# Kernel optimization log

Hardware: AMD Instinct MI355X
Metric: run time of the kernel (lower is better)

The kernel has to match this reference:

```python
import jax, jax.numpy as jnp
import numpy as np

B, S, T = 4, 512, 512
D, F, L, H, V = 512, 2048, 6, 8, 32000
HD = D // H


def setup_inputs() -> dict:
    key = jax.random.key(0)
    ks = list(jax.random.split(key, 16))
    it = iter(ks)

    def w(shape, scale=0.02):
        return jax.random.normal(next(it), shape, jnp.float32) * scale

    enc_in = jax.random.randint(next(it), (B, S), 0, V, dtype=jnp.int32)
    dec_in = jax.random.randint(next(it), (B, T), 0, V, dtype=jnp.int32)

    # sinusoidal positional encoding (make_sine_pos_encoding)
    pos = np.arange(S)[:, None].astype(np.float32)
    i = np.arange(D)[None, :].astype(np.float32)
    angle = pos / np.power(10000.0, (2.0 * np.floor(i / 2.0)) / D)
    pe = np.zeros((S, D), np.float32)
    pe[:, 0::2] = np.sin(angle[:, 0::2])
    pe[:, 1::2] = np.cos(angle[:, 1::2])

    return {
        "enc_in": enc_in,
        "dec_in": dec_in,
        "e_embed": w((V, D)),
        "d_embed": w((V, D)),
        "pos_enc": jnp.asarray(pe),
        "enc_mha_W": w((L, 4, D, D)),      # q,k,v,out
        "enc_mha_b": jnp.zeros((L, 4, D), jnp.float32),
        "enc_ln_g": jnp.ones((L, 2, D), jnp.float32),
        "enc_ln_b": jnp.zeros((L, 2, D), jnp.float32),
        "enc_ffn_W1": w((L, D, F)),
        "enc_ffn_b1": jnp.zeros((L, F), jnp.float32),
        "enc_ffn_W2": w((L, F, D)),
        "enc_ffn_b2": jnp.zeros((L, D), jnp.float32),
        "dec_mha_W": w((L, 8, D, D)),      # self q,k,v,out then cross q,k,v,out
        "dec_mha_b": jnp.zeros((L, 8, D), jnp.float32),
        "dec_ln_g": jnp.ones((L, 3, D), jnp.float32),
        "dec_ln_b": jnp.zeros((L, 3, D), jnp.float32),
        "dec_ffn_W1": w((L, D, F)),
        "dec_ffn_b1": jnp.zeros((L, F), jnp.float32),
        "dec_ffn_W2": w((L, F, D)),
        "dec_ffn_b2": jnp.zeros((L, D), jnp.float32),
    }


def _layer_norm(x, g, b, eps=1e-6):
    m = jnp.mean(x, axis=-1, keepdims=True)
    v = jnp.mean(jnp.square(x - m), axis=-1, keepdims=True)
    return (x - m) * jax.lax.rsqrt(v + eps) * g + b


def _split_heads(x):
    b, n, _ = x.shape
    return x.reshape(b, n, H, HD).transpose(0, 2, 1, 3)  # b h n d


def _mha(xq, xkv, W, b, mask):
    # W: [>=4, D, D] slice of (q,k,v,out); mask: broadcastable to [b,h,nq,nk]
    q = _split_heads(xq @ W[0] + b[0])
    k = _split_heads(xkv @ W[1] + b[1])
    v = _split_heads(xkv @ W[2] + b[2])
    s = jnp.einsum('bhqd,bhkd->bhqk', q, k) / jnp.sqrt(jnp.float32(HD))
    s = s + mask * (-1e9)
    a = jax.nn.softmax(s, axis=-1)
    o = jnp.einsum('bhqk,bhkd->bhqd', a, v)
    o = o.transpose(0, 2, 1, 3).reshape(xq.shape[0], xq.shape[1], D)
    return o @ W[3] + b[3]


def _forward(enc_in, dec_in, e_embed, d_embed, pos_enc,
             enc_mha_W, enc_mha_b, enc_ln_g, enc_ln_b,
             enc_ffn_W1, enc_ffn_b1, enc_ffn_W2, enc_ffn_b2,
             dec_mha_W, dec_mha_b, dec_ln_g, dec_ln_b,
             dec_ffn_W1, dec_ffn_b1, dec_ffn_W2, dec_ffn_b2):
    # masks: 1.0 where attention is blocked
    enc_pad = (enc_in == 0).astype(jnp.float32)[:, None, None, :]   # [B,1,1,S]
    dec_pad = (dec_in == 0).astype(jnp.float32)[:, None, None, :]   # [B,1,1,T]
    la = jnp.triu(jnp.ones((T, T), jnp.float32), k=1)[None, None]   # [1,1,T,T]
    look_ahead = jnp.maximum(la, dec_pad)                           # [B,1,T,T]

    scale = jnp.float32(D) ** 0.5
    e = e_embed[enc_in] * scale + pos_enc[None, :S]
    d = d_embed[dec_in] * scale + pos_enc[None, :T]

    for l in range(L):
        y = _mha(e, e, enc_mha_W[l], enc_mha_b[l], enc_pad)
        e = _layer_norm(e + y, enc_ln_g[l, 0], enc_ln_b[l, 0])
        y = jax.nn.relu(e @ enc_ffn_W1[l] + enc_ffn_b1[l]) @ enc_ffn_W2[l] + enc_ffn_b2[l]
        e = _layer_norm(e + y, enc_ln_g[l, 1], enc_ln_b[l, 1])

    for l in range(L):
        y = _mha(d, d, dec_mha_W[l, 0:4], dec_mha_b[l, 0:4], look_ahead)
        d = _layer_norm(d + y, dec_ln_g[l, 0], dec_ln_b[l, 0])
        y = _mha(d, e, dec_mha_W[l, 4:8], dec_mha_b[l, 4:8], enc_pad)
        d = _layer_norm(d + y, dec_ln_g[l, 1], dec_ln_b[l, 1])
        y = jax.nn.relu(d @ dec_ffn_W1[l] + dec_ffn_b1[l]) @ dec_ffn_W2[l] + dec_ffn_b2[l]
        d = _layer_norm(d + y, dec_ln_g[l, 2], dec_ln_b[l, 2])

    return d @ d_embed.T  # [B,T,V] logits


def reference(enc_in, dec_in, e_embed, d_embed, pos_enc,
              enc_mha_W, enc_mha_b, enc_ln_g, enc_ln_b,
              enc_ffn_W1, enc_ffn_b1, enc_ffn_W2, enc_ffn_b2,
              dec_mha_W, dec_mha_b, dec_ln_g, dec_ln_b,
              dec_ffn_W1, dec_ffn_b1, dec_ffn_W2, dec_ffn_b2):
    return _forward(enc_in, dec_in, e_embed, d_embed, pos_enc,
                    enc_mha_W, enc_mha_b, enc_ln_g, enc_ln_b,
                    enc_ffn_W1, enc_ffn_b1, enc_ffn_W2, enc_ffn_b2,
                    dec_mha_W, dec_mha_b, dec_ln_g, dec_ln_b,
                    dec_ffn_W1, dec_ffn_b1, dec_ffn_W2, dec_ffn_b2)
```

## Files before the change

kernel.cpp:

```cpp
#include <hip/hip_runtime.h>
#include <hip/hip_bf16.h>
#include <math.h>

#define B_ 4
#define S_ 512
#define D_ 512
#define F_ 2048
#define L_ 6
#define H_ 8
#define V_ 32000

typedef unsigned short u16;
typedef __attribute__((ext_vector_type(8))) short bhalf8;
typedef __attribute__((ext_vector_type(4))) float f32x4;

__device__ __forceinline__ u16 f2b(float v) {
    unsigned x = __builtin_bit_cast(unsigned, v);
    return (u16)((x + 0x7FFFu + ((x >> 16) & 1u)) >> 16);
}

#define GLD16(g, l) __builtin_amdgcn_global_load_lds( \
    (const __attribute__((address_space(1))) void*)(g), \
    (__attribute__((address_space(3))) void*)(l), 16, 0, 0)

__device__ __forceinline__ float redmax16(float v) {
    #pragma unroll
    for (int m = 1; m < 16; m <<= 1) v = fmaxf(v, __shfl_xor(v, m));
    return v;
}
__device__ __forceinline__ float redsum16(float v) {
    #pragma unroll
    for (int m = 1; m < 16; m <<= 1) v += __shfl_xor(v, m);
    return v;
}

template<int NWR, int NWC, int WM, int WN, int OUT, int RELU, int MLOOP,
         int SPLITA, int XMAJOR, int NT, int VTT, int SWZ>
__global__ __launch_bounds__(NWR * NWC * 64)
void mfma_gemm(const u16* __restrict__ A, const u16* __restrict__ A2, int acut,
               const u16* __restrict__ B,
               const float* __restrict__ bias, void* __restrict__ Cv,
               int K, int lda, int ldb, int ldc,
               u16* __restrict__ vtp, int vc0)
{
    constexpr int BM = NWR * WM, BN = NWC * WN;
    constexpr int NW = NWR * NWC;
    constexpr int CH_A = BM / 16, CH_B = BN / 16, CH = CH_A + CH_B;
    constexpr int NI = WM / 16, NJ = WN / 16;

    __shared__ u16 As[2][BM * 32];
    __shared__ u16 Bs[2][BN * 32];
    __shared__ u16 TT[VTT ? 64 * 72 : 8];

    const int tid = threadIdx.x;
    const int wid = tid >> 6, lane = tid & 63;
    const int wrow = wid / NWC, wcol = wid % NWC;
    long bn, bmbase;
    if (SWZ) {
        long b0 = blockIdx.x;
        long per = (long)gridDim.x >> 3;
        long w = (b0 & 7) * per + (b0 >> 3);
        bn = (w >> 4) * BN;
        bmbase = w & 15;
    } else {
        bn = (XMAJOR ? (long)blockIdx.y : (long)blockIdx.x) * BN;
        bmbase = (XMAJOR ? (long)blockIdx.x : (long)blockIdx.y);
    }
    const int r4 = lane >> 2, c4 = lane & 3;
    const int l15 = lane & 15, l4 = lane >> 4;

    const u16* Ause = (SPLITA && bn >= acut) ? A2 : A;

    #pragma unroll 1
    for (int mi = 0; mi < MLOOP; ++mi) {
        const long bm = (bmbase * MLOOP + mi) * BM;

        f32x4 acc[NI][NJ];
        #pragma unroll
        for (int i = 0; i < NI; ++i)
            #pragma unroll
            for (int j = 0; j < NJ; ++j)
                acc[i][j] = (f32x4){0.f, 0.f, 0.f, 0.f};

        #pragma unroll
        for (int t = 0; t < CH / NW; ++t) {
            int c = wid + t * NW;
            if (c < CH_A) {
                GLD16(Ause + (bm + c * 16 + r4) * (long)lda + c4 * 8,
                      &As[0][c * 512 + lane * 8]);
            } else {
                int cb = c - CH_A;
                GLD16(B + (bn + cb * 16 + r4) * (long)ldb + c4 * 8,
                      &Bs[0][cb * 512 + lane * 8]);
            }
        }

        for (int k0 = 0; k0 < K; k0 += 32) {
            const int cur = (k0 >> 5) & 1;
            __syncthreads();
            if (k0 + 32 < K) {
                const int kn = k0 + 32;
                #pragma unroll
                for (int t = 0; t < CH / NW; ++t) {
                    int c = wid + t * NW;
                    if (c < CH_A) {
                        GLD16(Ause + (bm + c * 16 + r4) * (long)lda + kn + c4 * 8,
                              &As[cur ^ 1][c * 512 + lane * 8]);
                    } else {
                        int cb = c - CH_A;
                        GLD16(B + (bn + cb * 16 + r4) * (long)ldb + kn + c4 * 8,
                              &Bs[cur ^ 1][cb * 512 + lane * 8]);
                    }
                }
            }
            bhalf8 af[NI], bfr[NJ];
            #pragma unroll
            for (int i = 0; i < NI; ++i)
                af[i] = *(const bhalf8*)&As[cur][(wrow * WM + i * 16 + l15) * 32 + l4 * 8];
            #pragma unroll
            for (int j = 0; j < NJ; ++j)
                bfr[j] = *(const bhalf8*)&Bs[cur][(wcol * WN + j * 16 + l15) * 32 + l4 * 8];
            #pragma unroll
            for (int i = 0; i < NI; ++i)
                #pragma unroll
                for (int j = 0; j < NJ; ++j)
                    acc[i][j] = __builtin_amdgcn_mfma_f32_16x16x32_bf16(af[i], bfr[j], acc[i][j], 0, 0, 0);
        }

        if (VTT && vtp != nullptr && bn >= vc0) {
            #pragma unroll
            for (int j = 0; j < NJ; ++j) {
                const int c = wcol * WN + j * 16 + l15;
                const float bv = bias ? bias[bn + c] : 0.f;
                #pragma unroll
                for (int i = 0; i < NI; ++i) {
                    const int rw = wrow * WM + i * 16 + (l4 << 2);
                    #pragma unroll
                    for (int r = 0; r < 4; ++r)
                        TT[c * 72 + rw + r] = f2b(acc[i][j][r] + bv);
                }
            }
            __syncthreads();
            {
                const int c = tid >> 1, hh = tid & 1;
                const u16* src = &TT[c * 72 + hh * 32];
                u16* dst = &vtp[(bn - vc0 + c) * 2048 + bm + hh * 32];
                #pragma unroll
                for (int p = 0; p < 4; ++p)
                    *(uint4*)(dst + p * 8) = *(const uint4*)(src + p * 8);
            }
            __syncthreads();
            continue;
        }

        float* Cf = (float*)Cv;
        u16*   Cb = (u16*)Cv;
        const int rowb = wrow * WM + (l4 << 2);
        const int colb = wcol * WN + l15;
        #pragma unroll
        for (int j = 0; j < NJ; ++j) {
            const long gc = bn + colb + j * 16;
            const float bv = bias ? bias[gc] : 0.f;
            #pragma unroll
            for (int i = 0; i < NI; ++i) {
                const long gr = bm + rowb + i * 16;
                #pragma unroll
                for (int r = 0; r < 4; ++r) {
                    float v = acc[i][j][r] + bv;
                    if (RELU) v = fmaxf(v, 0.f);
                    if (OUT == 0) {
                        if (NT) __builtin_nontemporal_store(v, &Cf[(gr + r) * (long)ldc + gc]);
                        else    Cf[(gr + r) * (long)ldc + gc] = v;
                    } else {
                        Cb[(gr + r) * (long)ldc + gc] = f2b(v);
                    }
                }
            }
        }
    }
}

__global__ __launch_bounds__(512)
void gemm_ln_kernel(const u16* __restrict__ A, const u16* __restrict__ B,
                    const float* __restrict__ bias,
                    float* __restrict__ x, u16* __restrict__ xb,
                    const float* __restrict__ g, const float* __restrict__ bb,
                    int K)
{
    __shared__ u16 As[16 * 32];
    __shared__ u16 Bs[512 * 32];
    __shared__ float red[2][16][8];
    __shared__ float mv[2][16];

    const int tid = threadIdx.x, w = tid >> 6, lane = tid & 63;
    const int l15 = lane & 15, l4 = lane >> 4;
    const int r4 = lane >> 2, c4 = lane & 3;
    const long bm = (long)blockIdx.x * 16;

    f32x4 acc[4];
    #pragma unroll
    for (int j = 0; j < 4; ++j) acc[j] = (f32x4){0.f, 0.f, 0.f, 0.f};

    for (int k0 = 0; k0 < K; k0 += 32) {
        #pragma unroll
        for (int t = 0; t < 5; ++t) {
            int c = w + t * 8;
            if (c < 33) {
                if (c == 0) {
                    GLD16(A + (bm + r4) * (long)K + k0 + c4 * 8, As + lane * 8);
                } else {
                    GLD16(B + ((c - 1) * 16 + r4) * (long)K + k0 + c4 * 8,
                          Bs + (c - 1) * 512 + lane * 8);
                }
            }
        }
        __syncthreads();
        bhalf8 af = *(const bhalf8*)&As[l15 * 32 + l4 * 8];
        #pragma unroll
        for (int j = 0; j < 4; ++j) {
            bhalf8 bf = *(const bhalf8*)&Bs[(w * 64 + j * 16 + l15) * 32 + l4 * 8];
            acc[j] = __builtin_amdgcn_mfma_f32_16x16x32_bf16(af, bf, acc[j], 0, 0, 0);
        }
        __syncthreads();
    }

    float vbuf[4][4], s[4] = {0, 0, 0, 0}, s2[4] = {0, 0, 0, 0};
    #pragma unroll
    for (int j = 0; j < 4; ++j) {
        int col = w * 64 + j * 16 + l15;
        float bv = bias[col];
        #pragma unroll
        for (int r = 0; r < 4; ++r) {
            int row = l4 * 4 + r;
            float v = acc[j][r] + bv + x[(bm + row) * 512 + col];
            vbuf[j][r] = v;
            s[r] += v; s2[r] += v * v;
        }
    }
    #pragma unroll
    for (int r = 0; r < 4; ++r) { s[r] = redsum16(s[r]); s2[r] = redsum16(s2[r]); }
    if (l15 == 0) {
        #pragma unroll
        for (int r = 0; r < 4; ++r) {
            red[0][l4 * 4 + r][w] = s[r];
            red[1][l4 * 4 + r][w] = s2[r];
        }
    }
    __syncthreads();
    if (tid < 16) {
        float S = 0.f, S2 = 0.f;
        #pragma unroll
        for (int q = 0; q < 8; ++q) { S += red[0][tid][q]; S2 += red[1][tid][q]; }
        float mean = S * (1.f / 512.f);
        float var = S2 * (1.f / 512.f) - mean * mean;
        mv[0][tid] = mean;
        mv[1][tid] = rsqrtf(var + 1e-6f);
    }
    __syncthreads();
    #pragma unroll
    for (int j = 0; j < 4; ++j) {
        int col = w * 64 + j * 16 + l15;
        float gg = g[col], bbv = bb[col];
        #pragma unroll
        for (int r = 0; r < 4; ++r) {
            int row = l4 * 4 + r;
            float o = (vbuf[j][r] - mv[0][row]) * mv[1][row] * gg + bbv;
            x[(bm + row) * 512 + col] = o;
            xb[(bm + row) * 512 + col] = f2b(o);
        }
    }
}

template<int CAUSAL>
__global__ __launch_bounds__(256)
void flash_kernel(const u16* __restrict__ Qp, int ldq,
                  const u16* __restrict__ Kp, int ldk,
                  const u16* __restrict__ Vt,
                  const int* __restrict__ tok,
                  u16* __restrict__ Op)
{
    __shared__ u16 QS[64 * 64];
    __shared__ u16 KS[2][64 * 64];
    __shared__ u16 VS[2][64 * 64];
    __shared__ u16 PS[4 * 16 * 64];
    __shared__ float MK[512];

    const int tid = threadIdx.x, lane = tid & 63, w = tid >> 6;
    const int l15 = lane & 15, l4 = lane >> 4;
    const int qb = blockIdx.x, bh = blockIdx.y;
    const int b = bh >> 3, h = bh & 7;

    const u16* Q = Qp + (long)(b * 512 + qb * 64) * ldq + h * 64;
    const u16* K = Kp + (long)(b * 512) * ldk + h * 64;
    const u16* V = Vt + (long)(h * 64) * 2048 + b * 512;
    u16* O = Op + (long)(b * 512 + qb * 64) * 512 + h * 64;

    {
        int t0 = tok[b * 512 + tid];
        int t1 = tok[b * 512 + 256 + tid];
        MK[tid]       = (t0 == 0) ? -1e9f : 0.f;
        MK[tid + 256] = (t1 == 0) ? -1e9f : 0.f;
    }
    const int r = tid >> 3;
    const int c = (tid & 7) ^ (r & 7);
    {
        GLD16(Q + (long)r * ldq + c * 8,        QS + tid * 8);
        GLD16(Q + (long)(r + 32) * ldq + c * 8, QS + 2048 + tid * 8);
        GLD16(K + (long)r * ldk + c * 8,              KS[0] + tid * 8);
        GLD16(K + (long)(32 + r) * ldk + c * 8,       KS[0] + 2048 + tid * 8);
        GLD16(V + (long)r * 2048 + c * 8,             VS[0] + tid * 8);
        GLD16(V + (long)(r + 32) * 2048 + c * 8,      VS[0] + 2048 + tid * 8);
    }
    __syncthreads();

    bhalf8 qa[2];
    #pragma unroll
    for (int kc = 0; kc < 2; ++kc) {
        int row = w * 16 + l15;
        qa[kc] = *(const bhalf8*)&QS[row * 64 + (((kc * 4 + l4) ^ (row & 7)) << 3)];
    }

    f32x4 oacc[4];
    float mrun[4], lrun[4];
    #pragma unroll
    for (int j = 0; j < 4; ++j) oacc[j] = (f32x4){0.f, 0.f, 0.f, 0.f};
    #pragma unroll
    for (int rr = 0; rr < 4; ++rr) { mrun[rr] = -1e30f; lrun[rr] = 0.f; }

    const int tmax = CAUSAL ? qb : 7;

    for (int t = 0; t <= tmax; ++t) {
        const int cur = t & 1;
        if (t < tmax) {
            const int tn = t + 1;
            GLD16(K + (long)(tn * 64 + r) * ldk + c * 8,        KS[cur ^ 1] + tid * 8);
            GLD16(K + (long)(tn * 64 + 32 + r) * ldk + c * 8,   KS[cur ^ 1] + 2048 + tid * 8);
            GLD16(V + (long)r * 2048 + tn * 64 + c * 8,         VS[cur ^ 1] + tid * 8);
            GLD16(V + (long)(r + 32) * 2048 + tn * 64 + c * 8,  VS[cur ^ 1] + 2048 + tid * 8);
        }
        f32x4 sac[4];
        #pragma unroll
        for (int jj = 0; jj < 4; ++jj) sac[jj] = (f32x4){0.f, 0.f, 0.f, 0.f};
        bhalf8 kf[4][2];
        #pragma unroll
        for (int jj = 0; jj < 4; ++jj)
            #pragma unroll
            for (int kc = 0; kc < 2; ++kc) {
                int row = jj * 16 + l15;
                kf[jj][kc] = *(const bhalf8*)&KS[cur][row * 64 + (((kc * 4 + l4) ^ (row & 7)) << 3)];
            }
        #pragma unroll
        for (int jj = 0; jj < 4; ++jj)
            #pragma unroll
            for (int kc = 0; kc < 2; ++kc)
                sac[jj] = __builtin_amdgcn_mfma_f32_16x16x32_bf16(qa[kc], kf[jj][kc], sac[jj], 0, 0, 0);

        #pragma unroll
        for (int jj = 0; jj < 4; ++jj) {
            float mk = MK[t * 64 + jj * 16 + l15];
            #pragma unroll
            for (int rr = 0; rr < 4; ++rr) {
                float mk2 = mk;
                if (CAUSAL && t == qb) {
                    int col = t * 64 + jj * 16 + l15;
                    int qr = qb * 64 + w * 16 + l4 * 4 + rr;
                    if (col > qr) mk2 = -1e9f;
                }
                sac[jj][rr] = sac[jj][rr] * 0.125f + mk2;
            }
        }
        #pragma unroll
        for (int rr = 0; rr < 4; ++rr) {
            float mx = fmaxf(fmaxf(sac[0][rr], sac[1][rr]), fmaxf(sac[2][rr], sac[3][rr]));
            mx = redmax16(mx);
            float mnew = fmaxf(mrun[rr], mx);
            float alpha = __expf(mrun[rr] - mnew);
            float sum = 0.f;
            int row_p = l4 * 4 + rr;
            #pragma unroll
            for (int jj = 0; jj < 4; ++jj) {
                float pv = __expf(sac[jj][rr] - mnew);
                sum += pv;
                int kv = jj * 16 + l15;
                PS[w * 1024 + row_p * 64 + ((((kv >> 3) ^ (row_p & 7)) << 3) | (kv & 7))] = f2b(pv);
            }
            sum = redsum16(sum);
            lrun[rr] = lrun[rr] * alpha + sum;
            mrun[rr] = mnew;
            #pragma unroll
            for (int jd = 0; jd < 4; ++jd) oacc[jd][rr] *= alpha;
        }
        bhalf8 pa[2], vf[4][2];
        #pragma unroll
        for (int kc = 0; kc < 2; ++kc) {
            int row = l15;
            pa[kc] = *(const bhalf8*)&PS[w * 1024 + row * 64 + (((kc * 4 + l4) ^ (row & 7)) << 3)];
        }
        #pragma unroll
        for (int jd = 0; jd < 4; ++jd)
            #pragma unroll
            for (int kc = 0; kc < 2; ++kc) {
                int row = jd * 16 + l15;
                vf[jd][kc] = *(const bhalf8*)&VS[cur][row * 64 + (((kc * 4 + l4) ^ (row & 7)) << 3)];
            }
        #pragma unroll
        for (int jd = 0; jd < 4; ++jd)
            #pragma unroll
            for (int kc = 0; kc < 2; ++kc)
                oacc[jd] = __builtin_amdgcn_mfma_f32_16x16x32_bf16(pa[kc], vf[jd][kc], oacc[jd], 0, 0, 0);
        __syncthreads();
    }

    #pragma unroll
    for (int rr = 0; rr < 4; ++rr) {
        float inv = 1.f / lrun[rr];
        int row = w * 16 + l4 * 4 + rr;
        #pragma unroll
        for (int jd = 0; jd < 4; ++jd)
            O[(long)row * 512 + jd * 16 + l15] = f2b(oacc[jd][rr] * inv);
    }
}

__global__ __launch_bounds__(256)
void transpose_many(const float* __restrict__ inA, const float* __restrict__ inB,
                    int zsplit, int R, int C, u16* __restrict__ out)
{
    int z = blockIdx.z;
    const float* in = (z < zsplit) ? inA + (long)z * R * C
                                   : inB + (long)(z - zsplit) * R * C;
    u16* o = out + (long)z * R * C;
    __shared__ float tb[64][65];
    const int tr = blockIdx.y * 64, tc = blockIdx.x * 64;
    const int col = threadIdx.x & 63, r0 = threadIdx.x >> 6;
    #pragma unroll
    for (int p = 0; p < 16; ++p) {
        int row = r0 * 16 + p;
        tb[row][col] = in[(long)(tr + row) * C + tc + col];
    }
    __syncthreads();
    #pragma unroll
    for (int p = 0; p < 16; ++p) {
        int row = r0 * 16 + p;
        o[(long)(tc + row) * R + tr + col] = f2b(tb[col][row]);
    }
}

__global__ __launch_bounds__(256)
void convert_b16(const float4* __restrict__ in, u16* __restrict__ out, long n4)
{
    long i = (long)blockIdx.x * 256 + threadIdx.x;
    if (i >= n4) return;
    float4 v = in[i];
    uint2 p;
    p.x = (unsigned)f2b(v.x) | ((unsigned)f2b(v.y) << 16);
    p.y = (unsigned)f2b(v.z) | ((unsigned)f2b(v.w) << 16);
    *(uint2*)(out + i * 4) = p;
}

__global__ __launch_bounds__(256)
void embed_kernel(const int* __restrict__ tE, const int* __restrict__ tD,
                  const float* __restrict__ eE, const float* __restrict__ eD,
                  const float* __restrict__ pos,
                  float* __restrict__ xE, float* __restrict__ xD,
                  u16* __restrict__ bE, u16* __restrict__ bD, float scale)
{
    const int z = blockIdx.y;
    const int* tok = z ? tD : tE;
    const float* emb = z ? eD : eE;
    float* x = z ? xD : xE;
    u16* xb = z ? bD : bE;
    int row = blockIdx.x;
    int s = row & (S_ - 1);
    int t = tok[row];
    const float* er = emb + (long)t * D_;
    const float* pr = pos + (long)s * D_;
    float* o = x + (long)row * D_;
    u16*  ob = xb + (long)row * D_;
    int i = threadIdx.x;
    float v0 = er[i]       * scale + pr[i];
    float v1 = er[i + 256] * scale + pr[i + 256];
    o[i] = v0;        o[i + 256] = v1;
    ob[i] = f2b(v0);  ob[i + 256] = f2b(v1);
}

__global__ __launch_bounds__(256)
void add_ln_kernel(float* __restrict__ x, const float* __restrict__ y,
                   u16* __restrict__ xb,
                   const float* __restrict__ g, const float* __restrict__ bb)
{
    long row = blockIdx.x;
    float* xr = x + row * D_;
    u16* xo = xb + row * D_;
    const float* yr = y + row * D_;
    int t = threadIdx.x, t2 = t + 256;

    float r0 = xr[t] + yr[t];
    float r1 = xr[t2] + yr[t2];
    float s = r0 + r1;
    float s2 = r0 * r0 + r1 * r1;
    #pragma unroll
    for (int i = 1; i < 64; i <<= 1) {
        s  += __shfl_xor(s, i);
        s2 += __shfl_xor(s2, i);
    }
    __shared__ float rs[4], rs2[4];
    int wid = t >> 6;
    if ((t & 63) == 0) { rs[wid] = s; rs2[wid] = s2; }
    __syncthreads();
    s  = rs[0] + rs[1] + rs[2] + rs[3];
    s2 = rs2[0] + rs2[1] + rs2[2] + rs2[3];

    float mean = s * (1.f / D_);
    float var  = s2 * (1.f / D_) - mean * mean;
    float inv  = rsqrtf(var + 1e-6f);
    float o0 = (r0 - mean) * inv * g[t]  + bb[t];
    float o1 = (r1 - mean) * inv * g[t2] + bb[t2];
    xr[t] = o0;       xr[t2] = o1;
    xo[t] = f2b(o0);  xo[t2] = f2b(o1);
}

extern "C" void kernel_launch(void* const* d_in, const int* in_sizes, int n_in,
                              void* d_out, int out_size, void* d_ws, size_t ws_size,
                              hipStream_t stream)
{
    const int*   enc_in     = (const int*)  d_in[0];
    const int*   dec_in     = (const int*)  d_in[1];
    const float* e_embed    = (const float*)d_in[2];
    const float* d_embed    = (const float*)d_in[3];
    const float* pos_enc    = (const float*)d_in[4];
    const float* enc_mha_W  = (const float*)d_in[5];
    const float* enc_mha_b  = (const float*)d_in[6];
    const float* enc_ln_g   = (const float*)d_in[7];
    const float* enc_ln_b   = (const float*)d_in[8];
    const float* enc_ffn_W1 = (const float*)d_in[9];
    const float* enc_ffn_b1 = (const float*)d_in[10];
    const float* enc_ffn_W2 = (const float*)d_in[11];
    const float* enc_ffn_b2 = (const float*)d_in[12];
    const float* dec_mha_W  = (const float*)d_in[13];
    const float* dec_mha_b  = (const float*)d_in[14];
    const float* dec_ln_g   = (const float*)d_in[15];
    const float* dec_ln_b   = (const float*)d_in[16];
    const float* dec_ffn_W1 = (const float*)d_in[17];
    const float* dec_ffn_b1 = (const float*)d_in[18];
    const float* dec_ffn_W2 = (const float*)d_in[19];
    const float* dec_ffn_b2 = (const float*)d_in[20];
    float* out = (float*)d_out;

    const int  BS  = B_ * S_;
    const long BSD = (long)BS * D_;
    const long DD  = (long)D_ * D_;
    const long DF  = (long)D_ * F_;

    char* p = (char*)d_ws;
    auto alloc = [&](long bytes) { char* r = p; p += (bytes + 255) & ~255L; return r; };
    float* e    = (float*)alloc(BSD * 4);
    float* dd   = (float*)alloc(BSD * 4);
    float* y    = (float*)alloc(BSD * 4);
    u16*   eb   = (u16*)  alloc(BSD * 2);
    u16*   ddb  = (u16*)  alloc(BSD * 2);
    u16*   qkv  = (u16*)  alloc((long)BS * 1536 * 2);
    u16*   att  = (u16*)  alloc(BSD * 2);
    u16*   vt   = (u16*)  alloc(BSD * 2);
    u16*   ffnh = (u16*)  alloc((long)BS * F_ * 2);
    u16*   wEmb = (u16*)  alloc((long)V_ * D_ * 2);
    u16*   wMha = (u16*)  alloc(72 * DD * 2);
    u16*   wF1  = (u16*)  alloc(12 * DF * 2);
    u16*   wF2  = (u16*)  alloc(12 * DF * 2);

    transpose_many<<<dim3(8, 8, 72), 256, 0, stream>>>(enc_mha_W, dec_mha_W, 24, 512, 512, wMha);
    transpose_many<<<dim3(32, 8, 12), 256, 0, stream>>>(enc_ffn_W1, dec_ffn_W1, 6, 512, 2048, wF1);
    transpose_many<<<dim3(8, 32, 12), 256, 0, stream>>>(enc_ffn_W2, dec_ffn_W2, 6, 2048, 512, wF2);
    convert_b16<<<16000, 256, 0, stream>>>((const float4*)d_embed, wEmb, (long)V_ * D_ / 4);

    const float scale = sqrtf((float)D_);
    embed_kernel<<<dim3(BS, 2), 256, 0, stream>>>(enc_in, dec_in, e_embed, d_embed,
                                                  pos_enc, e, dd, eb, ddb, scale);

    #define GEMM_BIG(grid, RELU, OUTT, A, Bp, bias, C, K, lda, ldb, ldc) \
        mfma_gemm<2,2,64,64,OUTT,RELU,1,0,0,0,0,0><<<grid, 256, 0, stream>>>(A, A, 1 << 30, Bp, bias, C, K, lda, ldb, ldc, nullptr, 0)
    #define GEMM_SKV(grid, A, Bp, bias, C, K, lda, ldb, ldc, vtp, vc0) \
        mfma_gemm<2,1,32,64,1,0,1,0,0,0,1,0><<<grid, 128, 0, stream>>>(A, A, 1 << 30, Bp, bias, C, K, lda, ldb, ldc, vtp, vc0)
    #define GEMM_SK(grid, OUTT, A, Bp, bias, C, K, lda, ldb, ldc) \
        mfma_gemm<2,1,32,64,OUTT,0,1,0,0,0,0,0><<<grid, 128, 0, stream>>>(A, A, 1 << 30, Bp, bias, C, K, lda, ldb, ldc, nullptr, 0)

    for (int l = 0; l < L_; ++l) {
        const u16* Wl = wMha + (long)l * 4 * DD;
        const float* bl = enc_mha_b + (long)l * 4 * D_;
        GEMM_SKV(dim3(24, 32), eb, Wl, bl, qkv, 512, 512, 512, 1536, vt, 1024);
        flash_kernel<0><<<dim3(8, 32), 256, 0, stream>>>(qkv, 1536, qkv + 512, 1536, vt, enc_in, att);
        gemm_ln_kernel<<<128, 512, 0, stream>>>(att, Wl + 3 * DD, bl + 3 * D_,
            e, eb, enc_ln_g + (long)(l * 2) * D_, enc_ln_b + (long)(l * 2) * D_, 512);
        GEMM_BIG(dim3(16, 16), 1, 1, eb, wF1 + (long)l * DF, enc_ffn_b1 + (long)l * F_,
                 ffnh, 512, 512, 512, 2048);
        GEMM_SK(dim3(8, 32), 0, ffnh, wF2 + (long)l * DF, enc_ffn_b2 + (long)l * D_,
                y, 2048, 2048, 2048, 512);
        add_ln_kernel<<<BS, 256, 0, stream>>>(e, y, eb,
            enc_ln_g + (long)(l * 2 + 1) * D_, enc_ln_b + (long)(l * 2 + 1) * D_);
    }

    for (int l = 0; l < L_; ++l) {
        const u16* Wl = wMha + (long)(24 + l * 8) * DD;
        const float* bl = dec_mha_b + (long)l * 8 * D_;
        GEMM_SKV(dim3(24, 32), ddb, Wl, bl, qkv, 512, 512, 512, 1536, vt, 1024);
        flash_kernel<1><<<dim3(8, 32), 256, 0, stream>>>(qkv, 1536, qkv + 512, 1536, vt, dec_in, att);
        gemm_ln_kernel<<<128, 512, 0, stream>>>(att, Wl + 3 * DD, bl + 3 * D_,
            dd, ddb, dec_ln_g + (long)(l * 3) * D_, dec_ln_b + (long)(l * 3) * D_, 512);
        mfma_gemm<2,1,32,64,1,0,1,1,0,0,1,0><<<dim3(24, 32), 128, 0, stream>>>(
            ddb, eb, 512, Wl + 4 * DD, bl + 4 * D_, qkv,
            512, 512, 512, 1536, vt, 1024);
        flash_kernel<0><<<dim3(8, 32), 256, 0, stream>>>(qkv, 1536, qkv + 512, 1536, vt, enc_in, att);
        gemm_ln_kernel<<<128, 512, 0, stream>>>(att, Wl + 7 * DD, bl + 7 * D_,
            dd, ddb, dec_ln_g + (long)(l * 3 + 1) * D_, dec_ln_b + (long)(l * 3 + 1) * D_, 512);
        GEMM_BIG(dim3(16, 16), 1, 1, ddb, wF1 + (long)(6 + l) * DF, dec_ffn_b1 + (long)l * F_,
                 ffnh, 512, 512, 512, 2048);
        GEMM_SK(dim3(8, 32), 0, ffnh, wF2 + (long)(6 + l) * DF, dec_ffn_b2 + (long)l * D_,
                y, 2048, 2048, 2048, 512);
        add_ln_kernel<<<BS, 256, 0, stream>>>(dd, y, ddb,
            dec_ln_g + (long)(l * 3 + 2) * D_, dec_ln_b + (long)(l * 3 + 2) * D_);
    }

    mfma_gemm<2,2,64,64,0,0,1,0,0,1,0,1><<<dim3(4000), 256, 0, stream>>>(
        ddb, ddb, 1 << 30, wEmb, nullptr, out, 512, 512, 512, 32000, nullptr, 0);
}
```

Before: 1.791 ms.

## Split-K FFN2 with bias folded into add-LN, smaller QKV tiles, MLOOP logits

```diff
diff --git a/kernel.cpp b/kernel.cpp
--- a/kernel.cpp
+++ b/kernel.cpp
@@ -35,22 +35,23 @@
 }
 
 template<int NWR, int NWC, int WM, int WN, int OUT, int RELU, int MLOOP,
-         int SPLITA, int XMAJOR, int NT, int VTT, int SWZ>
+         int SPLITA, int NT, int VTT, int SWZ>
 __global__ __launch_bounds__(NWR * NWC * 64)
 void mfma_gemm(const u16* __restrict__ A, const u16* __restrict__ A2, int acut,
                const u16* __restrict__ B,
                const float* __restrict__ bias, void* __restrict__ Cv,
                int K, int lda, int ldb, int ldc,
-               u16* __restrict__ vtp, int vc0)
+               u16* __restrict__ vtp, int vc0, long zoffC)
 {
     constexpr int BM = NWR * WM, BN = NWC * WN;
     constexpr int NW = NWR * NWC;
     constexpr int CH_A = BM / 16, CH_B = BN / 16, CH = CH_A + CH_B;
     constexpr int NI = WM / 16, NJ = WN / 16;
+    constexpr int TSTR = BM + 8;
 
     __shared__ u16 As[2][BM * 32];
     __shared__ u16 Bs[2][BN * 32];
-    __shared__ u16 TT[VTT ? 64 * 72 : 8];
+    __shared__ u16 TT[VTT ? 64 * TSTR : 8];
 
     const int tid = threadIdx.x;
     const int wid = tid >> 6, lane = tid & 63;
@@ -60,16 +61,20 @@
         long b0 = blockIdx.x;
         long per = (long)gridDim.x >> 3;
         long w = (b0 & 7) * per + (b0 >> 3);
-        bn = (w >> 4) * BN;
-        bmbase = w & 15;
+        constexpr int MB = 16 / MLOOP;
+        bn = (w / MB) * BN;
+        bmbase = w % MB;
     } else {
-        bn = (XMAJOR ? (long)blockIdx.y : (long)blockIdx.x) * BN;
-        bmbase = (XMAJOR ? (long)blockIdx.x : (long)blockIdx.y);
+        bn = (long)blockIdx.x * BN;
+        bmbase = (long)blockIdx.y;
     }
     const int r4 = lane >> 2, c4 = lane & 3;
     const int l15 = lane & 15, l4 = lane >> 4;
 
     const u16* Ause = (SPLITA && bn >= acut) ? A2 : A;
+    const long kz = (long)blockIdx.z * K;
+    Ause += kz;
+    B += kz;
 
     #pragma unroll 1
     for (int mi = 0; mi < MLOOP; ++mi) {
@@ -130,31 +135,31 @@
         if (VTT && vtp != nullptr && bn >= vc0) {
             #pragma unroll
             for (int j = 0; j < NJ; ++j) {
-                const int c = wcol * WN + j * 16 + l15;
-                const float bv = bias ? bias[bn + c] : 0.f;
+                const int cc = wcol * WN + j * 16 + l15;
+                const float bv = bias ? bias[bn + cc] : 0.f;
                 #pragma unroll
                 for (int i = 0; i < NI; ++i) {
                     const int rw = wrow * WM + i * 16 + (l4 << 2);
                     #pragma unroll
                     for (int r = 0; r < 4; ++r)
-                        TT[c * 72 + rw + r] = f2b(acc[i][j][r] + bv);
+                        TT[cc * TSTR + rw + r] = f2b(acc[i][j][r] + bv);
                 }
             }
             __syncthreads();
             {
-                const int c = tid >> 1, hh = tid & 1;
-                const u16* src = &TT[c * 72 + hh * 32];
-                u16* dst = &vtp[(bn - vc0 + c) * 2048 + bm + hh * 32];
+                const int cc = tid;
+                const u16* src = &TT[cc * TSTR];
+                u16* dst = &vtp[(bn - vc0 + cc) * 2048 + bm];
                 #pragma unroll
-                for (int p = 0; p < 4; ++p)
+                for (int p = 0; p < BM / 8; ++p)
                     *(uint4*)(dst + p * 8) = *(const uint4*)(src + p * 8);
             }
             __syncthreads();
             continue;
         }
 
-        float* Cf = (float*)Cv;
-        u16*   Cb = (u16*)Cv;
+        float* Cf = (float*)Cv + blockIdx.z * zoffC;
+        u16*   Cb = (u16*)Cv  + blockIdx.z * zoffC;
         const int rowb = wrow * WM + (l4 << 2);
         const int colb = wcol * WN + l15;
         #pragma unroll
@@ -484,18 +489,20 @@
 }
 
 __global__ __launch_bounds__(256)
-void add_ln_kernel(float* __restrict__ x, const float* __restrict__ y,
+void add_ln_kernel(float* __restrict__ x, const float* __restrict__ y0,
+                   const float* __restrict__ y1, const float* __restrict__ cb,
                    u16* __restrict__ xb,
                    const float* __restrict__ g, const float* __restrict__ bb)
 {
     long row = blockIdx.x;
     float* xr = x + row * D_;
     u16* xo = xb + row * D_;
-    const float* yr = y + row * D_;
+    const float* yr0 = y0 + row * D_;
+    const float* yr1 = y1 + row * D_;
     int t = threadIdx.x, t2 = t + 256;
 
-    float r0 = xr[t] + yr[t];
-    float r1 = xr[t2] + yr[t2];
+    float r0 = xr[t]  + yr0[t]  + yr1[t]  + cb[t];
+    float r1 = xr[t2] + yr0[t2] + yr1[t2] + cb[t2];
     float s = r0 + r1;
     float s2 = r0 * r0 + r1 * r1;
     #pragma unroll
@@ -555,7 +562,7 @@
     auto alloc = [&](long bytes) { char* r = p; p += (bytes + 255) & ~255L; return r; };
     float* e    = (float*)alloc(BSD * 4);
     float* dd   = (float*)alloc(BSD * 4);
-    float* y    = (float*)alloc(BSD * 4);
+    float* y    = (float*)alloc(2 * BSD * 4);
     u16*   eb   = (u16*)  alloc(BSD * 2);
     u16*   ddb  = (u16*)  alloc(BSD * 2);
     u16*   qkv  = (u16*)  alloc((long)BS * 1536 * 2);
@@ -576,49 +583,48 @@
     embed_kernel<<<dim3(BS, 2), 256, 0, stream>>>(enc_in, dec_in, e_embed, d_embed,
                                                   pos_enc, e, dd, eb, ddb, scale);
 
-    #define GEMM_BIG(grid, RELU, OUTT, A, Bp, bias, C, K, lda, ldb, ldc) \
-        mfma_gemm<2,2,64,64,OUTT,RELU,1,0,0,0,0,0><<<grid, 256, 0, stream>>>(A, A, 1 << 30, Bp, bias, C, K, lda, ldb, ldc, nullptr, 0)
-    #define GEMM_SKV(grid, A, Bp, bias, C, K, lda, ldb, ldc, vtp, vc0) \
-        mfma_gemm<2,1,32,64,1,0,1,0,0,0,1,0><<<grid, 128, 0, stream>>>(A, A, 1 << 30, Bp, bias, C, K, lda, ldb, ldc, vtp, vc0)
-    #define GEMM_SK(grid, OUTT, A, Bp, bias, C, K, lda, ldb, ldc) \
-        mfma_gemm<2,1,32,64,OUTT,0,1,0,0,0,0,0><<<grid, 128, 0, stream>>>(A, A, 1 << 30, Bp, bias, C, K, lda, ldb, ldc, nullptr, 0)
+    #define GEMM_SKV(A, Bp, bias, C) \
+        mfma_gemm<1,1,32,64,1,0,1,0,0,1,0><<<dim3(24, 64), 64, 0, stream>>>( \
+            A, A, 1 << 30, Bp, bias, C, 512, 512, 512, 1536, vt, 1024, 0)
+    #define GEMM_FFN1(A, Bp, bias, C) \
+        mfma_gemm<2,2,64,64,1,1,1,0,0,0,0><<<dim3(16, 16), 256, 0, stream>>>( \
+            A, A, 1 << 30, Bp, bias, C, 512, 512, 512, 2048, nullptr, 0, 0)
+    #define GEMM_FFN2(A, Bp) \
+        mfma_gemm<2,1,32,64,0,0,1,0,0,0,0><<<dim3(8, 32, 2), 128, 0, stream>>>( \
+            A, A, 1 << 30, Bp, nullptr, y, 1024, 2048, 2048, 512, nullptr, 0, BSD)
 
     for (int l = 0; l < L_; ++l) {
         const u16* Wl = wMha + (long)l * 4 * DD;
         const float* bl = enc_mha_b + (long)l * 4 * D_;
-        GEMM_SKV(dim3(24, 32), eb, Wl, bl, qkv, 512, 512, 512, 1536, vt, 1024);
+        GEMM_SKV(eb, Wl, bl, qkv);
         flash_kernel<0><<<dim3(8, 32), 256, 0, stream>>>(qkv, 1536, qkv + 512, 1536, vt, enc_in, att);
         gemm_ln_kernel<<<128, 512, 0, stream>>>(att, Wl + 3 * DD, bl + 3 * D_,
             e, eb, enc_ln_g + (long)(l * 2) * D_, enc_ln_b + (long)(l * 2) * D_, 512);
-        GEMM_BIG(dim3(16, 16), 1, 1, eb, wF1 + (long)l * DF, enc_ffn_b1 + (long)l * F_,
-                 ffnh, 512, 512, 512, 2048);
-        GEMM_SK(dim3(8, 32), 0, ffnh, wF2 + (long)l * DF, enc_ffn_b2 + (long)l * D_,
-                y, 2048, 2048, 2048, 512);
-        add_ln_kernel<<<BS, 256, 0, stream>>>(e, y, eb,
+        GEMM_FFN1(eb, wF1 + (long)l * DF, enc_ffn_b1 + (long)l * F_, ffnh);
+        GEMM_FFN2(ffnh, wF2 + (long)l * DF);
+        add_ln_kernel<<<BS, 256, 0, stream>>>(e, y, y + BSD, enc_ffn_b2 + (long)l * D_, eb,
             enc_ln_g + (long)(l * 2 + 1) * D_, enc_ln_b + (long)(l * 2 + 1) * D_);
     }
 
     for (int l = 0; l < L_; ++l) {
         const u16* Wl = wMha + (long)(24 + l * 8) * DD;
         const float* bl = dec_mha_b + (long)l * 8 * D_;
-        GEMM_SKV(dim3(24, 32), ddb, Wl, bl, qkv, 512, 512, 512, 1536, vt, 1024);
+        GEMM_SKV(ddb, Wl, bl, qkv);
         flash_kernel<1><<<dim3(8, 32), 256, 0, stream>>>(qkv, 1536, qkv + 512, 1536, vt, dec_in, att);
         gemm_ln_kernel<<<128, 512, 0, stream>>>(att, Wl + 3 * DD, bl + 3 * D_,
             dd, ddb, dec_ln_g + (long)(l * 3) * D_, dec_ln_b + (long)(l * 3) * D_, 512);
-        mfma_gemm<2,1,32,64,1,0,1,1,0,0,1,0><<<dim3(24, 32), 128, 0, stream>>>(
+        mfma_gemm<1,1,32,64,1,0,1,1,0,1,0><<<dim3(24, 64), 64, 0, stream>>>(
             ddb, eb, 512, Wl + 4 * DD, bl + 4 * D_, qkv,
-            512, 512, 512, 1536, vt, 1024);
+            512, 512, 512, 1536, vt, 1024, 0);
         flash_kernel<0><<<dim3(8, 32), 256, 0, stream>>>(qkv, 1536, qkv + 512, 1536, vt, enc_in, att);
         gemm_ln_kernel<<<128, 512, 0, stream>>>(att, Wl + 7 * DD, bl + 7 * D_,
             dd, ddb, dec_ln_g + (long)(l * 3 + 1) * D_, dec_ln_b + (long)(l * 3 + 1) * D_, 512);
-        GEMM_BIG(dim3(16, 16), 1, 1, ddb, wF1 + (long)(6 + l) * DF, dec_ffn_b1 + (long)l * F_,
-                 ffnh, 512, 512, 512, 2048);
-        GEMM_SK(dim3(8, 32), 0, ffnh, wF2 + (long)(6 + l) * DF, dec_ffn_b2 + (long)l * D_,
-                y, 2048, 2048, 2048, 512);
-        add_ln_kernel<<<BS, 256, 0, stream>>>(dd, y, ddb,
+        GEMM_FFN1(ddb, wF1 + (long)(6 + l) * DF, dec_ffn_b1 + (long)l * F_, ffnh);
+        GEMM_FFN2(ffnh, wF2 + (long)(6 + l) * DF);
+        add_ln_kernel<<<BS, 256, 0, stream>>>(dd, y, y + BSD, dec_ffn_b2 + (long)l * D_, ddb,
             dec_ln_g + (long)(l * 3 + 2) * D_, dec_ln_b + (long)(l * 3 + 2) * D_);
     }
 
-    mfma_gemm<2,2,64,64,0,0,1,0,0,1,0,1><<<dim3(4000), 256, 0, stream>>>(
-        ddb, ddb, 1 << 30, wEmb, nullptr, out, 512, 512, 512, 32000, nullptr, 0);
-}
+    mfma_gemm<2,2,64,64,0,0,2,0,1,0,1><<<dim3(2000), 256, 0, stream>>>(
+        ddb, ddb, 1 << 30, wEmb, nullptr, out, 512, 512, 512, 32000, nullptr, 0, 0);
+}
```

Result: faster. 1.689 ms (-5.7%).
